# Optimization experiments

Hardware: AMD Instinct MI355X
Metric: run time of the kernel (lower is better)

## Reference

```python
import jax, jax.numpy as jnp
import numpy as np

VOXEL_SIZE = np.array([0.1, 0.1, 0.2], np.float32)
PC_RANGE = np.array([-51.2, -51.2, -5.0, 51.2, 51.2, 3.0], np.float32)
MAX_POINTS = 32
MAX_VOXELS = 60000  # training cap (max_voxels[0])
GRID = np.round((PC_RANGE[3:] - PC_RANGE[:3]) / VOXEL_SIZE).astype(np.int64)  # [1024,1024,40]
N_POINTS = 1_200_000


def setup_inputs() -> dict:
    key = jax.random.key(0)
    k1, k2 = jax.random.split(key)
    lo = jnp.asarray(PC_RANGE[:3] - 2.0)   # slight margin -> some out-of-range points get dropped
    hi = jnp.asarray(PC_RANGE[3:] + 2.0)
    xyz = jax.random.uniform(k1, (N_POINTS, 3), minval=lo, maxval=hi)
    feat = jax.random.uniform(k2, (N_POINTS, 1))  # reflectivity
    return {"points": jnp.concatenate([xyz, feat], axis=1)}


def reference(points):
    # Hard voxelization (deterministic): first-occurrence voxel ordering,
    # first max_points points kept per voxel, capped at max_voxels.
    # Outputs padded to static MAX_VOXELS; voxel_num gives the valid count.
    N, ndim = points.shape
    gx, gy, gz = int(GRID[0]), int(GRID[1]), int(GRID[2])
    sentinel = gx * gy * gz  # flat id for out-of-range points (sorts last)

    vs = jnp.asarray(VOXEL_SIZE)
    rmin = jnp.asarray(PC_RANGE[:3])
    c = jnp.floor((points[:, :3] - rmin) / vs).astype(jnp.int32)  # [N,3] (x,y,z)
    valid = jnp.all((c >= 0) & (c < jnp.asarray(GRID, jnp.int32)), axis=1)
    flat = jnp.where(valid, (c[:, 0] * gy + c[:, 1]) * gz + c[:, 2], sentinel)

    # stable sort -> within a voxel, points keep original order
    order = jnp.argsort(flat, stable=True)
    sflat = flat[order]
    svalid = valid[order]

    new_seg = jnp.concatenate([jnp.array([True]), sflat[1:] != sflat[:-1]])
    seg_id = jnp.cumsum(new_seg) - 1                      # segment index per sorted point
    pos = jnp.arange(N)
    seg_start = jax.lax.cummax(jnp.where(new_seg, pos, 0), axis=0)
    rank = pos - seg_start                                # slot of point within its voxel

    seg_rep = jax.ops.segment_min(order, seg_id, num_segments=N)          # first-occurrence point idx
    seg_count = jax.ops.segment_sum(svalid.astype(jnp.int32), seg_id, num_segments=N)
    seg_exists = seg_count > 0                            # real (in-range) voxel segments

    # order voxels by first occurrence (matches deterministic CUDA kernel)
    rep_key = jnp.where(seg_exists, seg_rep, N)
    vox_order = jnp.argsort(rep_key, stable=True)
    vid = jnp.zeros(N, jnp.int32).at[vox_order].set(jnp.arange(N, dtype=jnp.int32))

    # scatter points into [MAX_VOXELS, MAX_POINTS, ndim]
    pv = vid[seg_id]
    keep = svalid & (pv < MAX_VOXELS) & (rank < MAX_POINTS)
    pv_s = jnp.where(keep, pv, MAX_VOXELS)  # OOB -> dropped
    voxels = jnp.zeros((MAX_VOXELS, MAX_POINTS, ndim), points.dtype)
    voxels = voxels.at[pv_s, jnp.minimum(rank, MAX_POINTS - 1)].set(points[order], mode='drop')

    # per-voxel outputs
    seg_vid = jnp.where(seg_exists, vid, MAX_VOXELS)
    npv = jnp.zeros(MAX_VOXELS, jnp.int32).at[seg_vid].set(
        jnp.minimum(seg_count, MAX_POINTS), mode='drop')
    seg_flat = jax.ops.segment_min(sflat, seg_id, num_segments=N)
    zc = seg_flat % gz
    yc = (seg_flat // gz) % gy
    xc = seg_flat // (gy * gz)
    coors = jnp.zeros((MAX_VOXELS, 3), jnp.int32).at[seg_vid].set(
        jnp.stack([zc, yc, xc], axis=1).astype(jnp.int32), mode='drop')  # (z, y, x) like mmcv

    voxel_num = jnp.minimum(jnp.sum(seg_exists.astype(jnp.int32)), MAX_VOXELS)
    return voxels, coors, npv, voxel_num
```

## Files before the change

kernel.cpp:

```cpp
#include <hip/hip_runtime.h>
#include <stdint.h>


#define GX 1024
#define GY 1024
#define GZ 40
#define MAXV 60000
#define MAXP 32
#define HBITS 21
#define HSIZE (1u << HBITS)
#define HMASK (HSIZE - 1u)
#define CANDBIT (1 << 30)
#define FLATMASK (CANDBIT - 1)
#define TB 256
#define KEARLY 131072
#define EMPTY64 0xFFFFFFFFFFFFFFFFull

#define OFF_COORS ((size_t)MAXV * MAXP * 4)
#define OFF_NPV   (OFF_COORS + (size_t)MAXV * 3)
#define OFF_VNUM  (OFF_NPV + (size_t)MAXV)

typedef unsigned long long u64;

__device__ __forceinline__ unsigned hashf(int flat) {
    return ((unsigned)flat * 2654435761u) >> (32 - HBITS);
}

__global__ void k_init(u64* __restrict__ h64, unsigned char* __restrict__ contested,
                       int* __restrict__ dupcnt, int* __restrict__ repidx,
                       int n, float* __restrict__ oF, int* __restrict__ nvox) {
    int i = blockIdx.x * blockDim.x + threadIdx.x;
    int stride = gridDim.x * blockDim.x;
    if (i == 0) *nvox = 0;
    for (int j = i; j < (int)HSIZE; j += stride) h64[j] = EMPTY64;
    int nw = (n + 3) / 4;
    unsigned* c4 = (unsigned*)contested;
    for (int j = i; j < nw; j += stride) c4[j] = 0;
    for (int j = i; j < MAXV; j += stride) { dupcnt[j] = 0; repidx[j] = -1; }
    for (int j = i; j < MAXV * 3; j += stride) oF[OFF_COORS + j] = 0.f;
}

__device__ __forceinline__ int voxel_flat(float4 pt) {
    float fx = floorf((pt.x + 51.2f) / 0.1f);
    float fy = floorf((pt.y + 51.2f) / 0.1f);
    float fz = floorf((pt.z + 5.0f) / 0.2f);
    int cx = (int)fx, cy = (int)fy, cz = (int)fz;
    bool valid = (fx >= 0.f) & (cx < GX) & (fy >= 0.f) & (cy < GY) & (fz >= 0.f) & (cz < GZ);
    return valid ? (cx * GY + cy) * GZ + cz : -1;
}

__device__ __forceinline__ int build_insert(int p, int flat, u64* __restrict__ h64,
                                            unsigned char* __restrict__ contested,
                                            int* __restrict__ nvox, int count_wins) {
    u64 want = ((u64)(unsigned)flat << 32) | (unsigned)p;
    unsigned slot = hashf(flat);
    int cand = 0, won = 0;
    for (int probe = 0; probe < 4096; probe++) {
        u64 cur = atomicCAS(&h64[slot], EMPTY64, want);
        if (cur == EMPTY64) { cand = 1; won = 1; break; }
        if ((unsigned)(cur >> 32) == (unsigned)flat) {
            if ((unsigned)cur > (unsigned)p) {
                u64 old = atomicMin(&h64[slot], want);
                unsigned oldrep = (unsigned)old;
                if (oldrep > (unsigned)p) {
                    contested[oldrep] = 1;
                    cand = 1;
                }
            }
            break;
        }
        slot = (slot + 1u) & HMASK;
    }
    if (count_wins && won) atomicAdd(nvox, 1);
    return flat | (cand ? CANDBIT : 0);
}

__global__ __launch_bounds__(TB) void k_build_early(const float4* __restrict__ pts, int nE,
                                                    u64* __restrict__ h64,
                                                    int* __restrict__ pflat,
                                                    unsigned char* __restrict__ contested,
                                                    int* __restrict__ nvox) {
    int p = blockIdx.x * blockDim.x + threadIdx.x;
    if (p >= nE) return;
    float4 pt = pts[p];
    int flat = voxel_flat(pt);
    if (flat < 0) { pflat[p] = -1; return; }
    pflat[p] = build_insert(p, flat, h64, contested, nvox, 1);
}

__global__ __launch_bounds__(TB) void k_build_late(const float4* __restrict__ pts, int n,
                                                   u64* __restrict__ h64,
                                                   int* __restrict__ pflat,
                                                   unsigned char* __restrict__ contested,
                                                   int* __restrict__ nvox) {
    int p = KEARLY + blockIdx.x * blockDim.x + threadIdx.x;
    if (p >= n) return;
    float4 pt = pts[p];
    int flat = voxel_flat(pt);
    if (flat < 0) { pflat[p] = -1; return; }
    if (*nvox >= MAXV) {
        unsigned slot = hashf(flat);
        int out = -1;
        for (int probe = 0; probe < 4096; probe++) {
            u64 cur = h64[slot];
            if (cur == EMPTY64) break;
            if ((unsigned)(cur >> 32) == (unsigned)flat) { out = flat; break; }
            slot = (slot + 1u) & HMASK;
        }
        pflat[p] = out;
        return;
    }
    pflat[p] = build_insert(p, flat, h64, contested, nvox, 0);
}

__global__ __launch_bounds__(TB) void k_flags(const int* __restrict__ pflat,
                                              const unsigned char* __restrict__ contested,
                                              int n, u64* __restrict__ flagbits,
                                              int* __restrict__ partials) {
    __shared__ int ws[4];
    int b = blockIdx.x, t = threadIdx.x;
    int i = b * TB + t;
    int pred = 0;
    if (i < n) {
        int pf = pflat[i];
        pred = (pf >= 0) && (pf & CANDBIT) && !contested[i];
    }
    u64 m = __ballot(pred);
    int w = t >> 6, lane = t & 63;
    if (lane == 0) { flagbits[b * 4 + w] = m; ws[w] = __popcll(m); }
    __syncthreads();
    if (t == 0) partials[b] = ws[0] + ws[1] + ws[2] + ws[3];
}

__global__ __launch_bounds__(1024) void k_scan(int* __restrict__ partials, int npart,
                                               float* __restrict__ oF) {
    __shared__ int sh[1024];
    int t = threadIdx.x;
    int v[5];
    int s = 0;
    #pragma unroll
    for (int k = 0; k < 5; k++) {
        int idx = t * 5 + k;
        v[k] = (idx < npart) ? partials[idx] : 0;
        s += v[k];
    }
    sh[t] = s;
    __syncthreads();
    for (int off = 1; off < 1024; off <<= 1) {
        int add = (t >= off) ? sh[t - off] : 0;
        __syncthreads();
        sh[t] += add;
        __syncthreads();
    }
    int run = sh[t] - s;
    #pragma unroll
    for (int k = 0; k < 5; k++) {
        int idx = t * 5 + k;
        if (idx < npart) partials[idx] = run;
        run += v[k];
    }
    if (t == 1023) {
        int total = sh[1023];
        if (total > MAXV) total = MAXV;
        oF[OFF_VNUM] = (float)total;
    }
}

__global__ __launch_bounds__(TB) void k_finish(const u64* __restrict__ flagbits,
                                               const int* __restrict__ partials,
                                               const int* __restrict__ pflat,
                                               const u64* __restrict__ h64,
                                               int* __restrict__ repidx,
                                               int* __restrict__ dupcnt,
                                               int* __restrict__ list, int n,
                                               float* __restrict__ oF) {
    int b = blockIdx.x, t = threadIdx.x;
    int i = b * TB + t;
    if (i >= n) return;
    int lane = t & 63, w = t >> 6;
    u64 w0 = flagbits[b * 4 + 0];
    u64 w1 = flagbits[b * 4 + 1];
    u64 w2 = flagbits[b * 4 + 2];
    u64 w3 = flagbits[b * 4 + 3];
    u64 myw = (w == 0) ? w0 : (w == 1) ? w1 : (w == 2) ? w2 : w3;
    int bit = (int)((myw >> lane) & 1);
    int pf = pflat[i];
    if (bit) {
        int wbase = (w > 0 ? __popcll(w0) : 0) + (w > 1 ? __popcll(w1) : 0)
                  + (w > 2 ? __popcll(w2) : 0);
        int vid = partials[b] + wbase + (int)__popcll(myw & ((1ull << lane) - 1ull));
        if (vid < MAXV) {
            int flat = pf & FLATMASK;
            int zc = flat % GZ;
            int t2 = flat / GZ;
            int yc = t2 % GY;
            int xc = t2 / GY;
            size_t cOff = OFF_COORS + (size_t)vid * 3;
            oF[cOff + 0] = (float)zc;
            oF[cOff + 1] = (float)yc;
            oF[cOff + 2] = (float)xc;
            repidx[vid] = i;
        }
    } else if (pf >= 0) {
        int flat = pf & FLATMASK;
        unsigned slot = hashf(flat);
        unsigned rep = 0xFFFFFFFFu;
        for (int probe = 0; probe < 4096; probe++) {
            u64 cur = h64[slot];
            if ((unsigned)(cur >> 32) == (unsigned)flat) { rep = (unsigned)cur; break; }
            if (cur == EMPTY64) break;
            slot = (slot + 1u) & HMASK;
        }
        if (rep != 0xFFFFFFFFu) {
            int br = (int)(rep >> 8);
            int lb = (int)(rep & 255u);
            int dvid = partials[br];
            int wb = br * 4, nw = lb >> 6;
            for (int q = 0; q < nw; q++) dvid += (int)__popcll(flagbits[wb + q]);
            int tail = lb & 63;
            if (tail) dvid += (int)__popcll(flagbits[wb + nw] & ((1ull << tail) - 1ull));
            if (dvid < MAXV) {
                int pos = atomicAdd(&dupcnt[dvid], 1);
                if (pos < MAXP - 1) list[dvid * (MAXP - 1) + pos] = i;
            }
        }
    }
}

__global__ __launch_bounds__(TB) void k_emit(const float4* __restrict__ pts,
                                             const int* __restrict__ repidx,
                                             const int* __restrict__ dupcnt,
                                             const int* __restrict__ list,
                                             float4* __restrict__ outVox,
                                             float* __restrict__ oF) {
    int gid = blockIdx.x * TB + threadIdx.x;
    int vid = gid >> 5;
    if (vid >= MAXV) return;
    int r = gid & 31;
    int ri = repidx[vid];
    int dc = dupcnt[vid];
    int d = dc < (MAXP - 1) ? dc : (MAXP - 1);
    int m = (ri >= 0) ? (1 + d) : 0;
    if (r == 0) oF[OFF_NPV + vid] = (float)m;
    float4 row = make_float4(0.f, 0.f, 0.f, 0.f);
    if (r == 0 && m > 0) {
        row = pts[ri];
    } else if (r < m) {
        const int* lst = &list[vid * (MAXP - 1)];
        int target = r - 1, pick = -1;
        for (int a = 0; a < d; a++) {
            int e = lst[a];
            int rk = 0;
            for (int bq = 0; bq < d; bq++) rk += (lst[bq] < e);
            if (rk == target) pick = e;
        }
        row = pts[pick];
    }
    outVox[(size_t)vid * MAXP + r] = row;
}

extern "C" void kernel_launch(void* const* d_in, const int* in_sizes, int n_in,
                              void* d_out, int out_size, void* d_ws, size_t ws_size,
                              hipStream_t stream) {
    int n = in_sizes[0] / 4;
    const float4* pts = (const float4*)d_in[0];

    int tb = TB;
    int nbp = (n + tb - 1) / tb;
    int nwords = nbp * 4;

    char* base = (char*)d_ws;
    size_t o = 0;
    int* partials = (int*)(base + o);  o += ((size_t)nbp * 4 + 255) & ~(size_t)255;
    int* dupcnt   = (int*)(base + o);  o += (size_t)MAXV * 4;
    int* repidx   = (int*)(base + o);  o += (size_t)MAXV * 4;
    o = (o + 255) & ~(size_t)255;
    u64* flagbits = (u64*)(base + o);  o += (size_t)nwords * 8;
    o = (o + 255) & ~(size_t)255;
    unsigned char* contested = (unsigned char*)(base + o);  o += ((size_t)n + 255) & ~(size_t)255;
    u64* h64      = (u64*)(base + o);  o += (size_t)HSIZE * 8;
    int* pflat    = (int*)(base + o);  o += (size_t)n * 4;
    int* list     = (int*)(base + o);  o += (size_t)MAXV * (MAXP - 1) * 4;
    o = (o + 255) & ~(size_t)255;
    int* nvox     = (int*)(base + o);  o += 256;

    float* oF = (float*)d_out;

    int nE = n < KEARLY ? n : KEARLY;
    int nbE = (nE + tb - 1) / tb;
    int nL = n - nE;

    k_init<<<2048, tb, 0, stream>>>(h64, contested, dupcnt, repidx, n, oF, nvox);
    k_build_early<<<nbE, tb, 0, stream>>>(pts, nE, h64, pflat, contested, nvox);
    if (nL > 0)
        k_build_late<<<(nL + tb - 1) / tb, tb, 0, stream>>>(pts, n, h64, pflat,
                                                            contested, nvox);
    k_flags<<<nbp, tb, 0, stream>>>(pflat, contested, n, flagbits, partials);
    k_scan<<<1, 1024, 0, stream>>>(partials, nbp, oF);
    k_finish<<<nbp, tb, 0, stream>>>(flagbits, partials, pflat, h64, repidx, dupcnt, list, n, oF);
    k_emit<<<(MAXV * MAXP + tb - 1) / tb, tb, 0, stream>>>(pts, repidx, dupcnt, list,
                                                           (float4*)d_out, oF);
}
```

Measured before the change: 135.1 us.

## Use occupancy bitmap and compacted duplicate list for late points once voxel cap hit

New measurement: 140.0 us. +3.6%, slower.

```diff
diff --git a/kernel.cpp b/kernel.cpp
--- a/kernel.cpp
+++ b/kernel.cpp
@@ -5,6 +5,7 @@
 #define GX 1024
 #define GY 1024
 #define GZ 40
+#define NVOXEL (GX * GY * GZ)
 #define MAXV 60000
 #define MAXP 32
 #define HBITS 21
@@ -14,6 +15,8 @@
 #define FLATMASK (CANDBIT - 1)
 #define TB 256
 #define KEARLY 131072
+#define NBE (KEARLY / TB)
+#define NBITW (NVOXEL / 32)
 #define EMPTY64 0xFFFFFFFFFFFFFFFFull
 
 #define OFF_COORS ((size_t)MAXV * MAXP * 4)
@@ -28,11 +31,13 @@
 
 __global__ void k_init(u64* __restrict__ h64, unsigned char* __restrict__ contested,
                        int* __restrict__ dupcnt, int* __restrict__ repidx,
-                       int n, float* __restrict__ oF, int* __restrict__ nvox) {
+                       int n, float* __restrict__ oF, int* __restrict__ nvox,
+                       unsigned* __restrict__ bitmap, unsigned* __restrict__ dcnt) {
     int i = blockIdx.x * blockDim.x + threadIdx.x;
     int stride = gridDim.x * blockDim.x;
-    if (i == 0) *nvox = 0;
+    if (i == 0) { *nvox = 0; *dcnt = 0; }
     for (int j = i; j < (int)HSIZE; j += stride) h64[j] = EMPTY64;
+    for (int j = i; j < NBITW; j += stride) bitmap[j] = 0u;
     int nw = (n + 3) / 4;
     unsigned* c4 = (unsigned*)contested;
     for (int j = i; j < nw; j += stride) c4[j] = 0;
@@ -51,7 +56,9 @@
 
 __device__ __forceinline__ int build_insert(int p, int flat, u64* __restrict__ h64,
                                             unsigned char* __restrict__ contested,
-                                            int* __restrict__ nvox, int count_wins) {
+                                            int* __restrict__ nvox,
+                                            unsigned* __restrict__ bitmap,
+                                            int count_wins) {
     u64 want = ((u64)(unsigned)flat << 32) | (unsigned)p;
     unsigned slot = hashf(flat);
     int cand = 0, won = 0;
@@ -71,7 +78,10 @@
         }
         slot = (slot + 1u) & HMASK;
     }
-    if (count_wins && won) atomicAdd(nvox, 1);
+    if (won) {
+        atomicOr(&bitmap[(unsigned)flat >> 5], 1u << (flat & 31));
+        if (count_wins) atomicAdd(nvox, 1);
+    }
     return flat | (cand ? CANDBIT : 0);
 }
 
@@ -79,49 +89,53 @@
                                                     u64* __restrict__ h64,
                                                     int* __restrict__ pflat,
                                                     unsigned char* __restrict__ contested,
-                                                    int* __restrict__ nvox) {
+                                                    int* __restrict__ nvox,
+                                                    unsigned* __restrict__ bitmap) {
     int p = blockIdx.x * blockDim.x + threadIdx.x;
     if (p >= nE) return;
     float4 pt = pts[p];
     int flat = voxel_flat(pt);
     if (flat < 0) { pflat[p] = -1; return; }
-    pflat[p] = build_insert(p, flat, h64, contested, nvox, 1);
+    pflat[p] = build_insert(p, flat, h64, contested, nvox, bitmap, 1);
 }
 
 __global__ __launch_bounds__(TB) void k_build_late(const float4* __restrict__ pts, int n,
                                                    u64* __restrict__ h64,
                                                    int* __restrict__ pflat,
                                                    unsigned char* __restrict__ contested,
-                                                   int* __restrict__ nvox) {
+                                                   int* __restrict__ nvox,
+                                                   unsigned* __restrict__ bitmap,
+                                                   u64* __restrict__ latedup,
+                                                   unsigned* __restrict__ dcnt) {
     int p = KEARLY + blockIdx.x * blockDim.x + threadIdx.x;
     if (p >= n) return;
     float4 pt = pts[p];
     int flat = voxel_flat(pt);
-    if (flat < 0) { pflat[p] = -1; return; }
-    if (*nvox >= MAXV) {
-        unsigned slot = hashf(flat);
-        int out = -1;
-        for (int probe = 0; probe < 4096; probe++) {
-            u64 cur = h64[slot];
-            if (cur == EMPTY64) break;
-            if ((unsigned)(cur >> 32) == (unsigned)flat) { out = flat; break; }
-            slot = (slot + 1u) & HMASK;
-        }
-        pflat[p] = out;
+    if (*nvox < MAXV) {
+        if (flat < 0) { pflat[p] = -1; return; }
+        pflat[p] = build_insert(p, flat, h64, contested, nvox, bitmap, 0);
         return;
     }
-    pflat[p] = build_insert(p, flat, h64, contested, nvox, 0);
+    if (flat < 0) return;
+    unsigned w = bitmap[(unsigned)flat >> 5];
+    if (w & (1u << (flat & 31))) {
+        unsigned pos = atomicAdd(dcnt, 1u);
+        if (pos < (unsigned)(n - KEARLY))
+            latedup[pos] = ((u64)(unsigned)flat << 32) | (unsigned)p;
+    }
 }
 
 __global__ __launch_bounds__(TB) void k_flags(const int* __restrict__ pflat,
                                               const unsigned char* __restrict__ contested,
                                               int n, u64* __restrict__ flagbits,
-                                              int* __restrict__ partials) {
+                                              int* __restrict__ partials,
+                                              const int* __restrict__ nvox) {
     __shared__ int ws[4];
     int b = blockIdx.x, t = threadIdx.x;
     int i = b * TB + t;
+    int fastmode = (*nvox >= MAXV);
     int pred = 0;
-    if (i < n) {
+    if (i < n && (b < NBE || !fastmode)) {
         int pf = pflat[i];
         pred = (pf >= 0) && (pf & CANDBIT) && !contested[i];
     }
@@ -166,6 +180,34 @@
     }
 }
 
+__device__ __forceinline__ void register_dup(int flat, int i,
+                                             const u64* __restrict__ h64,
+                                             const u64* __restrict__ flagbits,
+                                             const int* __restrict__ partials,
+                                             int* __restrict__ dupcnt,
+                                             int* __restrict__ list) {
+    unsigned slot = hashf(flat);
+    unsigned rep = 0xFFFFFFFFu;
+    for (int probe = 0; probe < 4096; probe++) {
+        u64 cur = h64[slot];
+        if ((unsigned)(cur >> 32) == (unsigned)flat) { rep = (unsigned)cur; break; }
+        if (cur == EMPTY64) break;
+        slot = (slot + 1u) & HMASK;
+    }
+    if (rep == 0xFFFFFFFFu) return;
+    int br = (int)(rep >> 8);
+    int lb = (int)(rep & 255u);
+    int dvid = partials[br];
+    int wb = br * 4, nw = lb >> 6;
+    for (int q = 0; q < nw; q++) dvid += (int)__popcll(flagbits[wb + q]);
+    int tail = lb & 63;
+    if (tail) dvid += (int)__popcll(flagbits[wb + nw] & ((1ull << tail) - 1ull));
+    if (dvid < MAXV) {
+        int pos = atomicAdd(&dupcnt[dvid], 1);
+        if (pos < MAXP - 1) list[dvid * (MAXP - 1) + pos] = i;
+    }
+}
+
 __global__ __launch_bounds__(TB) void k_finish(const u64* __restrict__ flagbits,
                                                const int* __restrict__ partials,
                                                const int* __restrict__ pflat,
@@ -173,8 +215,24 @@
                                                int* __restrict__ repidx,
                                                int* __restrict__ dupcnt,
                                                int* __restrict__ list, int n,
-                                               float* __restrict__ oF) {
+                                               float* __restrict__ oF,
+                                               const int* __restrict__ nvox,
+                                               const u64* __restrict__ latedup,
+                                               const unsigned* __restrict__ dcnt) {
     int b = blockIdx.x, t = threadIdx.x;
+    int fastmode = (*nvox >= MAXV);
+    if (fastmode && b >= NBE) {
+        unsigned cnt = *dcnt;
+        unsigned cap = (unsigned)(n - KEARLY);
+        if (cnt > cap) cnt = cap;
+        unsigned idx = (unsigned)(b - NBE) * TB + t;
+        if (idx < cnt) {
+            u64 e = latedup[idx];
+            register_dup((int)(e >> 32), (int)(unsigned)e,
+                         h64, flagbits, partials, dupcnt, list);
+        }
+        return;
+    }
     int i = b * TB + t;
     if (i >= n) return;
     int lane = t & 63, w = t >> 6;
@@ -202,28 +260,7 @@
             repidx[vid] = i;
         }
     } else if (pf >= 0) {
-        int flat = pf & FLATMASK;
-        unsigned slot = hashf(flat);
-        unsigned rep = 0xFFFFFFFFu;
-        for (int probe = 0; probe < 4096; probe++) {
-            u64 cur = h64[slot];
-            if ((unsigned)(cur >> 32) == (unsigned)flat) { rep = (unsigned)cur; break; }
-            if (cur == EMPTY64) break;
-            slot = (slot + 1u) & HMASK;
-        }
-        if (rep != 0xFFFFFFFFu) {
-            int br = (int)(rep >> 8);
-            int lb = (int)(rep & 255u);
-            int dvid = partials[br];
-            int wb = br * 4, nw = lb >> 6;
-            for (int q = 0; q < nw; q++) dvid += (int)__popcll(flagbits[wb + q]);
-            int tail = lb & 63;
-            if (tail) dvid += (int)__popcll(flagbits[wb + nw] & ((1ull << tail) - 1ull));
-            if (dvid < MAXV) {
-                int pos = atomicAdd(&dupcnt[dvid], 1);
-                if (pos < MAXP - 1) list[dvid * (MAXP - 1) + pos] = i;
-            }
-        }
+        register_dup(pf & FLATMASK, i, h64, flagbits, partials, dupcnt, list);
     }
 }
 
@@ -282,7 +319,12 @@
     int* pflat    = (int*)(base + o);  o += (size_t)n * 4;
     int* list     = (int*)(base + o);  o += (size_t)MAXV * (MAXP - 1) * 4;
     o = (o + 255) & ~(size_t)255;
+    unsigned* bitmap = (unsigned*)(base + o);  o += (size_t)NBITW * 4;
+    o = (o + 255) & ~(size_t)255;
+    u64* latedup  = (u64*)(base + o);  o += (size_t)(n > KEARLY ? n - KEARLY : 1) * 8;
+    o = (o + 255) & ~(size_t)255;
     int* nvox     = (int*)(base + o);  o += 256;
+    unsigned* dcnt = (unsigned*)(base + o);  o += 256;
 
     float* oF = (float*)d_out;
 
@@ -290,14 +332,17 @@
     int nbE = (nE + tb - 1) / tb;
     int nL = n - nE;
 
-    k_init<<<2048, tb, 0, stream>>>(h64, contested, dupcnt, repidx, n, oF, nvox);
-    k_build_early<<<nbE, tb, 0, stream>>>(pts, nE, h64, pflat, contested, nvox);
+    k_init<<<2048, tb, 0, stream>>>(h64, contested, dupcnt, repidx, n, oF, nvox,
+                                    bitmap, dcnt);
+    k_build_early<<<nbE, tb, 0, stream>>>(pts, nE, h64, pflat, contested, nvox, bitmap);
     if (nL > 0)
         k_build_late<<<(nL + tb - 1) / tb, tb, 0, stream>>>(pts, n, h64, pflat,
-                                                            contested, nvox);
-    k_flags<<<nbp, tb, 0, stream>>>(pflat, contested, n, flagbits, partials);
+                                                            contested, nvox, bitmap,
+                                                            latedup, dcnt);
+    k_flags<<<nbp, tb, 0, stream>>>(pflat, contested, n, flagbits, partials, nvox);
     k_scan<<<1, 1024, 0, stream>>>(partials, nbp, oF);
-    k_finish<<<nbp, tb, 0, stream>>>(flagbits, partials, pflat, h64, repidx, dupcnt, list, n, oF);
+    k_finish<<<nbp, tb, 0, stream>>>(flagbits, partials, pflat, h64, repidx, dupcnt,
+                                     list, n, oF, nvox, latedup, dcnt);
     k_emit<<<(MAXV * MAXP + tb - 1) / tb, tb, 0, stream>>>(pts, repidx, dupcnt, list,
                                                            (float4*)d_out, oF);
 }
```
